# Kernel optimization log

Measured on AMD Instinct MI355X. Metric: run time of the kernel, lower is better.

The kernel has to match this reference:

```python
import jax, jax.numpy as jnp
import numpy as np

D_MODEL = 1024
D_Q = 1024
D_V = 1024


def setup_inputs() -> dict:
    key = jax.random.key(0)
    k0, k1, k2, k3 = jax.random.split(key, 4)
    embedding_word = jax.random.normal(k0, (4, 2048, D_MODEL), dtype=jnp.float32)
    # nn.Linear weights are [out, in]; we store transposed [in, out] for x @ W
    s = 1.0 / np.sqrt(D_MODEL)
    w_q = jax.random.uniform(k1, (D_MODEL, D_Q), jnp.float32, -s, s)
    w_k = jax.random.uniform(k2, (D_MODEL, D_Q), jnp.float32, -s, s)
    w_v = jax.random.uniform(k3, (D_MODEL, D_V), jnp.float32, -s, s)
    return {"embedding_word": embedding_word, "w_q": w_q, "w_k": w_k, "w_v": w_v}


def reference(embedding_word, w_q, w_k, w_v):
    # q,k: [B,T,d_q]; v: [B,T,d_v]
    q = embedding_word @ w_q
    k = embedding_word @ w_k
    v = embedding_word @ w_v
    scores = jnp.einsum("btd,bsd->bts", q, k)  # [B,T,T]
    T = scores.shape[-1]
    causal = jnp.tril(jnp.ones((T, T), dtype=bool))  # True = keep
    masked = jnp.where(causal, scores, -jnp.inf)
    weights = jax.nn.softmax(masked / jnp.sqrt(jnp.float32(D_Q)), axis=-1)
    return jnp.einsum("bts,bsv->btv", weights, v)
```

## Files before the change

kernel.cpp:

```cpp
#include <hip/hip_runtime.h>
#include <cstdint>

typedef __bf16 bf16_t;
typedef __attribute__((ext_vector_type(8))) __bf16 bf16x8;
typedef __attribute__((ext_vector_type(4))) __bf16 bf16x4;
typedef __attribute__((ext_vector_type(4))) float f32x4;

#define AS1 __attribute__((address_space(1)))
#define AS3 __attribute__((address_space(3)))

template <typename OutT>
__global__ __launch_bounds__(256)
void gemm_nt(const bf16_t* __restrict__ A, const bf16_t* __restrict__ B,
             OutT* __restrict__ C, int K, int lda, int ldb, int ldc)
{
  const int bm = blockIdx.y, bn = blockIdx.x;
  const int m0 = bm * 128, n0 = bn * 128;

  __shared__ bf16_t As[2][128 * 64];
  __shared__ bf16_t Bs[2][128 * 64];

  const int tid = threadIdx.x;
  const int wave = tid >> 6, lane = tid & 63;
  const int lm = lane & 15, qd = lane >> 4;
  const int wm = (wave >> 1) * 64, wn = (wave & 1) * 64;

  const int rowl = lane >> 3;
  const int q = (lane & 7) ^ rowl;
  const bf16_t* Abase = A + (long)(m0 + wave * 8 + rowl) * lda + q * 8;
  const bf16_t* Bbase = B + (long)(n0 + wave * 8 + rowl) * ldb + q * 8;
  const int woff = wave * 512;

  auto stage = [&](int k0, int b) {
#pragma unroll
    for (int i = 0; i < 4; i++) {
      __builtin_amdgcn_global_load_lds((const AS1 void*)(Abase + (long)i * 32 * lda + k0),
                                       (AS3 void*)(As[b] + woff + i * 2048), 16, 0, 0);
      __builtin_amdgcn_global_load_lds((const AS1 void*)(Bbase + (long)i * 32 * ldb + k0),
                                       (AS3 void*)(Bs[b] + woff + i * 2048), 16, 0, 0);
    }
  };

  f32x4 acc[4][4] = {};

  stage(0, 0);
  int buf = 0;
  for (int k0 = 0; k0 < K; k0 += 64) {
    __syncthreads();
    if (k0 + 64 < K) stage(k0 + 64, buf ^ 1);
#pragma unroll
    for (int s = 0; s < 2; s++) {
      bf16x8 aF[4], bF[4];
#pragma unroll
      for (int i = 0; i < 4; i++) {
        const int r = wm + i * 16 + lm;
        aF[i] = *(const bf16x8*)&As[buf][r * 64 + (((s * 4 + qd) ^ (lm & 7)) << 3)];
      }
#pragma unroll
      for (int j = 0; j < 4; j++) {
        const int r = wn + j * 16 + lm;
        bF[j] = *(const bf16x8*)&Bs[buf][r * 64 + (((s * 4 + qd) ^ (lm & 7)) << 3)];
      }
#pragma unroll
      for (int i = 0; i < 4; i++)
#pragma unroll
        for (int j = 0; j < 4; j++)
          acc[i][j] = __builtin_amdgcn_mfma_f32_16x16x32_bf16(aF[i], bF[j], acc[i][j], 0, 0, 0);
    }
    buf ^= 1;
  }

#pragma unroll
  for (int i = 0; i < 4; i++) {
    const int row = m0 + wm + i * 16 + qd * 4;
#pragma unroll
    for (int j = 0; j < 4; j++) {
      const int col = n0 + wn + j * 16 + lm;
#pragma unroll
      for (int r = 0; r < 4; r++)
        C[(long)(row + r) * ldc + col] = (OutT)acc[i][j][r];
    }
  }
}

template <typename OutT>
__global__ __launch_bounds__(256)
void gemm_nt64(const bf16_t* __restrict__ A, const bf16_t* __restrict__ B,
               OutT* __restrict__ C, int K, int lda, int ldb, int ldc,
               long sA, long sB, long sC, int causalHalf, int kLimit64)
{
  int bm = blockIdx.y;
  const int bn = blockIdx.x;
  if (kLimit64) bm = gridDim.y - 1 - bm;
  if (causalHalf && bn > (bm >> 1)) return;
  A += (long)blockIdx.z * sA;
  B += (long)blockIdx.z * sB;
  C += (long)blockIdx.z * sC;
  const int m0 = bm * 64, n0 = bn * 128;
  int Keff = K;
  if (kLimit64) { const int kl = ((bm >> 1) + 1) * 128; if (kl < Keff) Keff = kl; }

  __shared__ bf16_t As[64 * 64];
  __shared__ bf16_t Bs[128 * 64];

  const int tid = threadIdx.x;
  const int wave = tid >> 6, lane = tid & 63;
  const int lm = lane & 15, qd = lane >> 4;
  const int wn = wave * 32;

  const int rowl = lane >> 3;
  const int q = (lane & 7) ^ rowl;
  const bf16_t* Abase = A + (long)(m0 + wave * 8 + rowl) * lda + q * 8;
  const bf16_t* Bbase = B + (long)(n0 + wave * 8 + rowl) * ldb + q * 8;
  const int woff = wave * 512;

  f32x4 acc[4][2] = {};

  for (int k0 = 0; k0 < Keff; k0 += 64) {
#pragma unroll
    for (int i = 0; i < 2; i++)
      __builtin_amdgcn_global_load_lds((const AS1 void*)(Abase + (long)i * 32 * lda + k0),
                                       (AS3 void*)(As + woff + i * 2048), 16, 0, 0);
#pragma unroll
    for (int i = 0; i < 4; i++)
      __builtin_amdgcn_global_load_lds((const AS1 void*)(Bbase + (long)i * 32 * ldb + k0),
                                       (AS3 void*)(Bs + woff + i * 2048), 16, 0, 0);
    __syncthreads();
#pragma unroll
    for (int s = 0; s < 2; s++) {
      bf16x8 aF[4], bF[2];
#pragma unroll
      for (int i = 0; i < 4; i++) {
        const int r = i * 16 + lm;
        aF[i] = *(const bf16x8*)&As[r * 64 + (((s * 4 + qd) ^ (lm & 7)) << 3)];
      }
#pragma unroll
      for (int j = 0; j < 2; j++) {
        const int r = wn + j * 16 + lm;
        bF[j] = *(const bf16x8*)&Bs[r * 64 + (((s * 4 + qd) ^ (lm & 7)) << 3)];
      }
#pragma unroll
      for (int i = 0; i < 4; i++)
#pragma unroll
        for (int j = 0; j < 2; j++)
          acc[i][j] = __builtin_amdgcn_mfma_f32_16x16x32_bf16(aF[i], bF[j], acc[i][j], 0, 0, 0);
    }
    __syncthreads();
  }

#pragma unroll
  for (int i = 0; i < 4; i++) {
    const int row = m0 + i * 16 + qd * 4;
#pragma unroll
    for (int j = 0; j < 2; j++) {
      const int col = n0 + wn + j * 16 + lm;
#pragma unroll
      for (int r = 0; r < 4; r++)
        C[(long)(row + r) * ldc + col] = (OutT)acc[i][j][r];
    }
  }
}

__global__ void cvt_f32_bf16(const float* __restrict__ in, bf16_t* __restrict__ out, int n4)
{
  const int i = blockIdx.x * blockDim.x + threadIdx.x;
  if (i >= n4) return;
  const float4 f = ((const float4*)in)[i];
  bf16x4 o = {(bf16_t)f.x, (bf16_t)f.y, (bf16_t)f.z, (bf16_t)f.w};
  ((bf16x4*)out)[i] = o;
}

__global__ void cvt_transpose_w(const float* __restrict__ wq, const float* __restrict__ wk,
                                const float* __restrict__ wv, bf16_t* __restrict__ WT)
{
  const float* W = (blockIdx.z == 0) ? wq : (blockIdx.z == 1) ? wk : wv;
  bf16_t* O = WT + (long)blockIdx.z * 1024 * 1024;
  __shared__ float tile[32][33];
  const int x = blockIdx.x * 32 + threadIdx.x;
  const int y = blockIdx.y * 32 + threadIdx.y;
  tile[threadIdx.y][threadIdx.x] = W[(long)y * 1024 + x];
  __syncthreads();
  const int ox = blockIdx.x * 32 + threadIdx.y;
  const int oy = blockIdx.y * 32 + threadIdx.x;
  O[(long)ox * 1024 + oy] = (bf16_t)tile[threadIdx.x][threadIdx.y];
}

__global__ __launch_bounds__(256)
void softmax_causal(bf16_t* __restrict__ S)
{
  const int row = blockIdx.x;
  const int t = row & 2047;
  const int kend = ((t >> 7) + 1) << 7;
  bf16_t* Sr = S + (long)row * 2048;
  const int base = threadIdx.x * 8;

  uint4 u = {0, 0, 0, 0};
  if (base <= t) u = *(const uint4*)(Sr + base);
  const unsigned short* up = (const unsigned short*)&u;
  float v[8];
  float m = -3.0e38f;
#pragma unroll
  for (int j = 0; j < 8; j++) {
    const float x = __uint_as_float(((unsigned)up[j]) << 16);
    v[j] = (base + j <= t) ? x : -3.0e38f;
    m = fmaxf(m, v[j]);
  }
#pragma unroll
  for (int off = 32; off > 0; off >>= 1) m = fmaxf(m, __shfl_xor(m, off));
  __shared__ float redm[4], redl[4];
  const int wave = threadIdx.x >> 6, lane = threadIdx.x & 63;
  if (lane == 0) redm[wave] = m;
  __syncthreads();
  m = fmaxf(fmaxf(redm[0], redm[1]), fmaxf(redm[2], redm[3]));

  float p[8], l = 0.f;
#pragma unroll
  for (int j = 0; j < 8; j++) {
    p[j] = (base + j <= t) ? __expf((v[j] - m) * 0.03125f) : 0.f;
    l += p[j];
  }
#pragma unroll
  for (int off = 32; off > 0; off >>= 1) l += __shfl_xor(l, off);
  if (lane == 0) redl[wave] = l;
  __syncthreads();
  l = (redl[0] + redl[1]) + (redl[2] + redl[3]);
  const float rl = 1.0f / l;

  if (base < kend) {
    uint4 w;
    unsigned* wp = (unsigned*)&w;
#pragma unroll
    for (int h = 0; h < 4; h++) {
      bf16_t a = (bf16_t)(p[2 * h] * rl);
      bf16_t b = (bf16_t)(p[2 * h + 1] * rl);
      wp[h] = (unsigned)__builtin_bit_cast(unsigned short, a) |
              ((unsigned)__builtin_bit_cast(unsigned short, b) << 16);
    }
    *(uint4*)(Sr + base) = w;
  }
}

extern "C" void kernel_launch(void* const* d_in, const int* in_sizes, int n_in,
                              void* d_out, int out_size, void* d_ws, size_t ws_size,
                              hipStream_t stream)
{
  const float* X  = (const float*)d_in[0];
  const float* Wq = (const float*)d_in[1];
  const float* Wk = (const float*)d_in[2];
  const float* Wv = (const float*)d_in[3];
  float* out = (float*)d_out;

  char* p = (char*)d_ws;
  bf16_t* QK = (bf16_t*)p;  p += (size_t)8192 * 2048 * 2;
  bf16_t* VT = (bf16_t*)p;  p += (size_t)1024 * 8192 * 2;
  bf16_t* WT = (bf16_t*)p;  p += (size_t)3072 * 1024 * 2;
  bf16_t* Xb = (bf16_t*)p;
  bf16_t* S  = (bf16_t*)p;

  cvt_f32_bf16<<<8192, 256, 0, stream>>>(X, Xb, 8388608 / 4);
  cvt_transpose_w<<<dim3(32, 32, 3), dim3(32, 32), 0, stream>>>(Wq, Wk, Wv, WT);
  gemm_nt<bf16_t><<<dim3(16, 64), 256, 0, stream>>>(
      Xb, WT, QK, 1024, 1024, 1024, 2048);
  gemm_nt<bf16_t><<<dim3(64, 8), 256, 0, stream>>>(
      WT + (long)2048 * 1024, Xb, VT, 1024, 1024, 1024, 8192);
  gemm_nt64<bf16_t><<<dim3(16, 32, 4), 256, 0, stream>>>(
      QK, QK + 1024, S, 1024, 2048, 2048, 2048,
      (long)2048 * 2048, (long)2048 * 2048, (long)2048 * 2048, 1, 0);
  softmax_causal<<<8192, 256, 0, stream>>>(S);
  gemm_nt64<float><<<dim3(8, 32, 4), 256, 0, stream>>>(
      S, VT, out, 2048, 2048, 8192, 1024,
      (long)2048 * 2048, 2048, (long)2048 * 1024, 0, 1);
}
```

Measured before the change: 253.3 us.

## Merge projection GEMMs into one launch and double-buffer the 64-row GEMM

The QK and V projection GEMMs are combined into a single 1536-block kernel that picks its operands from the block index. This removes one launch and the tail between the two grids. The attention GEMM kernel (gemm_nt64) now double-buffers its shared-memory tiles, so the next K tile loads while MFMAs run on the current one, and one barrier per iteration is dropped. The cost is twice the LDS per block for gemm_nt64 (48KB), which may lower occupancy.

New measurement: 278.9 us. 1.1x slower.

```diff
diff --git a/kernel.cpp b/kernel.cpp
--- a/kernel.cpp
+++ b/kernel.cpp
@@ -9,13 +9,23 @@
 #define AS1 __attribute__((address_space(1)))
 #define AS3 __attribute__((address_space(3)))
 
-template <typename OutT>
 __global__ __launch_bounds__(256)
-void gemm_nt(const bf16_t* __restrict__ A, const bf16_t* __restrict__ B,
-             OutT* __restrict__ C, int K, int lda, int ldb, int ldc)
-{
-  const int bm = blockIdx.y, bn = blockIdx.x;
-  const int m0 = bm * 128, n0 = bn * 128;
+void gemm_proj(const bf16_t* __restrict__ Xb, const bf16_t* __restrict__ WT,
+               bf16_t* __restrict__ QK, bf16_t* __restrict__ VT)
+{
+  int id = blockIdx.x;
+  const bf16_t *A, *B;
+  bf16_t* C;
+  int ldc, m0, n0;
+  if (id < 1024) {
+    A = Xb; B = WT; C = QK; ldc = 2048;
+    m0 = (id >> 4) * 128; n0 = (id & 15) * 128;
+  } else {
+    id -= 1024;
+    A = WT + 2 * 1024 * 1024; B = Xb; C = VT; ldc = 8192;
+    m0 = (id >> 6) * 128; n0 = (id & 63) * 128;
+  }
+  const int lda = 1024, ldb = 1024, K = 1024;
 
   __shared__ bf16_t As[2][128 * 64];
   __shared__ bf16_t Bs[2][128 * 64];
@@ -78,7 +88,7 @@
       const int col = n0 + wn + j * 16 + lm;
 #pragma unroll
       for (int r = 0; r < 4; r++)
-        C[(long)(row + r) * ldc + col] = (OutT)acc[i][j][r];
+        C[(long)(row + r) * ldc + col] = (bf16_t)acc[i][j][r];
     }
   }
 }
@@ -100,8 +110,8 @@
   int Keff = K;
   if (kLimit64) { const int kl = ((bm >> 1) + 1) * 128; if (kl < Keff) Keff = kl; }
 
-  __shared__ bf16_t As[64 * 64];
-  __shared__ bf16_t Bs[128 * 64];
+  __shared__ bf16_t As[2][64 * 64];
+  __shared__ bf16_t Bs[2][128 * 64];
 
   const int tid = threadIdx.x;
   const int wave = tid >> 6, lane = tid & 63;
@@ -114,30 +124,36 @@
   const bf16_t* Bbase = B + (long)(n0 + wave * 8 + rowl) * ldb + q * 8;
   const int woff = wave * 512;
 
-  f32x4 acc[4][2] = {};
-
-  for (int k0 = 0; k0 < Keff; k0 += 64) {
+  auto stage = [&](int k0, int b) {
 #pragma unroll
     for (int i = 0; i < 2; i++)
       __builtin_amdgcn_global_load_lds((const AS1 void*)(Abase + (long)i * 32 * lda + k0),
-                                       (AS3 void*)(As + woff + i * 2048), 16, 0, 0);
+                                       (AS3 void*)(As[b] + woff + i * 2048), 16, 0, 0);
 #pragma unroll
     for (int i = 0; i < 4; i++)
       __builtin_amdgcn_global_load_lds((const AS1 void*)(Bbase + (long)i * 32 * ldb + k0),
-                                       (AS3 void*)(Bs + woff + i * 2048), 16, 0, 0);
+                                       (AS3 void*)(Bs[b] + woff + i * 2048), 16, 0, 0);
+  };
+
+  f32x4 acc[4][2] = {};
+
+  stage(0, 0);
+  int buf = 0;
+  for (int k0 = 0; k0 < Keff; k0 += 64) {
     __syncthreads();
+    if (k0 + 64 < Keff) stage(k0 + 64, buf ^ 1);
 #pragma unroll
     for (int s = 0; s < 2; s++) {
       bf16x8 aF[4], bF[2];
 #pragma unroll
       for (int i = 0; i < 4; i++) {
         const int r = i * 16 + lm;
-        aF[i] = *(const bf16x8*)&As[r * 64 + (((s * 4 + qd) ^ (lm & 7)) << 3)];
+        aF[i] = *(const bf16x8*)&As[buf][r * 64 + (((s * 4 + qd) ^ (lm & 7)) << 3)];
       }
 #pragma unroll
       for (int j = 0; j < 2; j++) {
         const int r = wn + j * 16 + lm;
-        bF[j] = *(const bf16x8*)&Bs[r * 64 + (((s * 4 + qd) ^ (lm & 7)) << 3)];
+        bF[j] = *(const bf16x8*)&Bs[buf][r * 64 + (((s * 4 + qd) ^ (lm & 7)) << 3)];
       }
 #pragma unroll
       for (int i = 0; i < 4; i++)
@@ -145,7 +161,7 @@
         for (int j = 0; j < 2; j++)
           acc[i][j] = __builtin_amdgcn_mfma_f32_16x16x32_bf16(aF[i], bF[j], acc[i][j], 0, 0, 0);
     }
-    __syncthreads();
+    buf ^= 1;
   }
 
 #pragma unroll
@@ -259,10 +275,7 @@
 
   cvt_f32_bf16<<<8192, 256, 0, stream>>>(X, Xb, 8388608 / 4);
   cvt_transpose_w<<<dim3(32, 32, 3), dim3(32, 32), 0, stream>>>(Wq, Wk, Wv, WT);
-  gemm_nt<bf16_t><<<dim3(16, 64), 256, 0, stream>>>(
-      Xb, WT, QK, 1024, 1024, 1024, 2048);
-  gemm_nt<bf16_t><<<dim3(64, 8), 256, 0, stream>>>(
-      WT + (long)2048 * 1024, Xb, VT, 1024, 1024, 1024, 8192);
+  gemm_proj<<<1536, 256, 0, stream>>>(Xb, WT, QK, VT);
   gemm_nt64<bf16_t><<<dim3(16, 32, 4), 256, 0, stream>>>(
       QK, QK + 1024, S, 1024, 2048, 2048, 2048,
       (long)2048 * 2048, (long)2048 * 2048, (long)2048 * 2048, 1, 0);
```

## Double-buffer LDS tiles in gemm_nt64 and merge prep kernels into one launch

Applied to the files above, without the earlier changes.

gemm_nt64 now keeps two LDS buffers for A and B. It issues the next tile's global-to-LDS loads right after the barrier, so memory fetches overlap the MFMA work, and one of the two barriers per iteration is dropped. The separate bf16 conversion and weight-transpose kernels are merged into a single prep launch, and the transpose uses 256-thread blocks that each handle four rows. This costs twice the LDS in gemm_nt64, which can lower occupancy, and relies on a single barrier per iteration to keep buffer reuse correct.

Measured after the change: 248.7 us. About the same (-1.8%).

```diff
diff --git a/kernel.cpp b/kernel.cpp
--- a/kernel.cpp
+++ b/kernel.cpp
@@ -100,8 +100,8 @@
   int Keff = K;
   if (kLimit64) { const int kl = ((bm >> 1) + 1) * 128; if (kl < Keff) Keff = kl; }
 
-  __shared__ bf16_t As[64 * 64];
-  __shared__ bf16_t Bs[128 * 64];
+  __shared__ bf16_t As[2][64 * 64];
+  __shared__ bf16_t Bs[2][128 * 64];
 
   const int tid = threadIdx.x;
   const int wave = tid >> 6, lane = tid & 63;
@@ -114,30 +114,36 @@
   const bf16_t* Bbase = B + (long)(n0 + wave * 8 + rowl) * ldb + q * 8;
   const int woff = wave * 512;
 
-  f32x4 acc[4][2] = {};
-
-  for (int k0 = 0; k0 < Keff; k0 += 64) {
+  auto stage = [&](int k0, int b) {
 #pragma unroll
     for (int i = 0; i < 2; i++)
       __builtin_amdgcn_global_load_lds((const AS1 void*)(Abase + (long)i * 32 * lda + k0),
-                                       (AS3 void*)(As + woff + i * 2048), 16, 0, 0);
+                                       (AS3 void*)(As[b] + woff + i * 2048), 16, 0, 0);
 #pragma unroll
     for (int i = 0; i < 4; i++)
       __builtin_amdgcn_global_load_lds((const AS1 void*)(Bbase + (long)i * 32 * ldb + k0),
-                                       (AS3 void*)(Bs + woff + i * 2048), 16, 0, 0);
+                                       (AS3 void*)(Bs[b] + woff + i * 2048), 16, 0, 0);
+  };
+
+  f32x4 acc[4][2] = {};
+
+  stage(0, 0);
+  int buf = 0;
+  for (int k0 = 0; k0 < Keff; k0 += 64) {
     __syncthreads();
+    if (k0 + 64 < Keff) stage(k0 + 64, buf ^ 1);
 #pragma unroll
     for (int s = 0; s < 2; s++) {
       bf16x8 aF[4], bF[2];
 #pragma unroll
       for (int i = 0; i < 4; i++) {
         const int r = i * 16 + lm;
-        aF[i] = *(const bf16x8*)&As[r * 64 + (((s * 4 + qd) ^ (lm & 7)) << 3)];
+        aF[i] = *(const bf16x8*)&As[buf][r * 64 + (((s * 4 + qd) ^ (lm & 7)) << 3)];
       }
 #pragma unroll
       for (int j = 0; j < 2; j++) {
         const int r = wn + j * 16 + lm;
-        bF[j] = *(const bf16x8*)&Bs[r * 64 + (((s * 4 + qd) ^ (lm & 7)) << 3)];
+        bF[j] = *(const bf16x8*)&Bs[buf][r * 64 + (((s * 4 + qd) ^ (lm & 7)) << 3)];
       }
 #pragma unroll
       for (int i = 0; i < 4; i++)
@@ -145,7 +151,7 @@
         for (int j = 0; j < 2; j++)
           acc[i][j] = __builtin_amdgcn_mfma_f32_16x16x32_bf16(aF[i], bF[j], acc[i][j], 0, 0, 0);
     }
-    __syncthreads();
+    buf ^= 1;
   }
 
 #pragma unroll
@@ -161,28 +167,39 @@
   }
 }
 
-__global__ void cvt_f32_bf16(const float* __restrict__ in, bf16_t* __restrict__ out, int n4)
-{
-  const int i = blockIdx.x * blockDim.x + threadIdx.x;
-  if (i >= n4) return;
-  const float4 f = ((const float4*)in)[i];
-  bf16x4 o = {(bf16_t)f.x, (bf16_t)f.y, (bf16_t)f.z, (bf16_t)f.w};
-  ((bf16x4*)out)[i] = o;
-}
-
-__global__ void cvt_transpose_w(const float* __restrict__ wq, const float* __restrict__ wk,
-                                const float* __restrict__ wv, bf16_t* __restrict__ WT)
-{
-  const float* W = (blockIdx.z == 0) ? wq : (blockIdx.z == 1) ? wk : wv;
-  bf16_t* O = WT + (long)blockIdx.z * 1024 * 1024;
+__global__ __launch_bounds__(256)
+void prep(const float* __restrict__ X, bf16_t* __restrict__ Xb,
+          const float* __restrict__ wq, const float* __restrict__ wk,
+          const float* __restrict__ wv, bf16_t* __restrict__ WT)
+{
+  const int b = blockIdx.x;
+  if (b < 8192) {
+    const int i = b * 256 + threadIdx.x;
+    const float4 f = ((const float4*)X)[i];
+    bf16x4 o = {(bf16_t)f.x, (bf16_t)f.y, (bf16_t)f.z, (bf16_t)f.w};
+    ((bf16x4*)Xb)[i] = o;
+    return;
+  }
+  const int wid = b - 8192;
+  const int z = wid >> 10;
+  const int t = wid & 1023;
+  const int tix = t & 31, tiy = t >> 5;
+  const float* W = (z == 0) ? wq : (z == 1) ? wk : wv;
+  bf16_t* O = WT + (long)z * 1024 * 1024;
+
   __shared__ float tile[32][33];
-  const int x = blockIdx.x * 32 + threadIdx.x;
-  const int y = blockIdx.y * 32 + threadIdx.y;
-  tile[threadIdx.y][threadIdx.x] = W[(long)y * 1024 + x];
+  const int x = threadIdx.x & 31, y0 = threadIdx.x >> 5;
+#pragma unroll
+  for (int r = 0; r < 4; r++) {
+    const int y = y0 + r * 8;
+    tile[y][x] = W[(long)(tiy * 32 + y) * 1024 + (tix * 32 + x)];
+  }
   __syncthreads();
-  const int ox = blockIdx.x * 32 + threadIdx.y;
-  const int oy = blockIdx.y * 32 + threadIdx.x;
-  O[(long)ox * 1024 + oy] = (bf16_t)tile[threadIdx.x][threadIdx.y];
+#pragma unroll
+  for (int r = 0; r < 4; r++) {
+    const int y = y0 + r * 8;
+    O[(long)(tix * 32 + y) * 1024 + (tiy * 32 + x)] = (bf16_t)tile[x][y];
+  }
 }
 
 __global__ __launch_bounds__(256)
@@ -257,8 +274,7 @@
   bf16_t* Xb = (bf16_t*)p;
   bf16_t* S  = (bf16_t*)p;
 
-  cvt_f32_bf16<<<8192, 256, 0, stream>>>(X, Xb, 8388608 / 4);
-  cvt_transpose_w<<<dim3(32, 32, 3), dim3(32, 32), 0, stream>>>(Wq, Wk, Wv, WT);
+  prep<<<8192 + 3072, 256, 0, stream>>>(X, Xb, Wq, Wk, Wv, WT);
   gemm_nt<bf16_t><<<dim3(16, 64), 256, 0, stream>>>(
       Xb, WT, QK, 1024, 1024, 1024, 2048);
   gemm_nt<bf16_t><<<dim3(64, 8), 256, 0, stream>>>(
```
